# Optimization experiments

Measured on AMD Instinct MI355X. Metric: run time of the kernel, lower is better.

The kernel has to match this reference:

```python
import jax, jax.numpy as jnp
import numpy as np

NUM_LAYERS = 2
SHAPES = [(100, 100), (50, 50), (25, 25), (13, 13)]  # (H, W) per level
D, NH, NP, NL = 256, 8, 4, 4
DH = D // NH
DFF = 1024
B = 2
S = sum(h * w for h, w in SHAPES)  # 13294


def layer_norm(x, g, b, eps=1e-5):
    m = x.mean(-1, keepdims=True)
    v = jnp.var(x, axis=-1, keepdims=True)
    return (x - m) * jax.lax.rsqrt(v + eps) * g + b


def get_reference_points(valid_ratios):
    refs = []
    for lvl, (H_, W_) in enumerate(SHAPES):
        ry, rx = jnp.meshgrid(jnp.linspace(0.5, H_ - 0.5, H_),
                              jnp.linspace(0.5, W_ - 0.5, W_), indexing='ij')
        ry = ry.reshape(-1)[None] / (valid_ratios[:, None, lvl, 1] * H_)
        rx = rx.reshape(-1)[None] / (valid_ratios[:, None, lvl, 0] * W_)
        refs.append(jnp.stack([rx, ry], -1))
    ref = jnp.concatenate(refs, 1)                      # [B, S, 2]
    return ref[:, :, None] * valid_ratios[:, None]      # [B, S, NL, 2]


def sample_level(value_l, H_, W_, loc):
    # value_l: [B, nH, H*W, Dh]; loc: [B, Q, nH, P, 2] normalized in [0,1]
    x = loc[..., 0] * W_ - 0.5
    y = loc[..., 1] * H_ - 0.5
    x0 = jnp.floor(x)
    y0 = jnp.floor(y)
    Bq, Q = loc.shape[0], loc.shape[1]
    acc = 0.
    corners = ((x0, y0, (x0 + 1 - x) * (y0 + 1 - y)),
               (x0 + 1, y0, (x - x0) * (y0 + 1 - y)),
               (x0, y0 + 1, (x0 + 1 - x) * (y - y0)),
               (x0 + 1, y0 + 1, (x - x0) * (y - y0)))
    for xi, yi, w in corners:  # zero-padding grid_sample: invalid corners contribute 0
        valid = (xi >= 0) & (xi <= W_ - 1) & (yi >= 0) & (yi <= H_ - 1)
        idx = (jnp.clip(yi, 0, H_ - 1) * W_ + jnp.clip(xi, 0, W_ - 1)).astype(jnp.int32)
        idx = jnp.transpose(idx, (0, 2, 1, 3)).reshape(Bq, NH, Q * NP)
        g = jnp.take_along_axis(value_l, idx[..., None], axis=2)  # [B,nH,Q*P,Dh]
        wv = jnp.transpose((w * valid).astype(value_l.dtype), (0, 2, 1, 3)).reshape(Bq, NH, Q * NP)
        acc = acc + g * wv[..., None]
    return acc.reshape(Bq, NH, Q, NP, DH)


def msda(query, ref, src, W_val, b_val, W_off, b_off, W_attn, b_attn, W_out, b_out):
    Bq, Q = query.shape[:2]
    value = (src @ W_val + b_val).reshape(Bq, S, NH, DH)
    off = (query @ W_off + b_off).reshape(Bq, Q, NH, NL, NP, 2)
    attn = jax.nn.softmax((query @ W_attn + b_attn).reshape(Bq, Q, NH, NL * NP), -1)
    attn = attn.reshape(Bq, Q, NH, NL, NP)
    normalizer = jnp.array([[w, h] for h, w in SHAPES], dtype=query.dtype)  # [NL,2] (x,y)
    loc = ref[:, :, None, :, None, :] + off / normalizer[None, None, None, :, None, :]
    out = jnp.zeros((Bq, NH, Q, DH), query.dtype)
    start = 0
    for l, (H_, W_) in enumerate(SHAPES):
        v_l = jnp.transpose(value[:, start:start + H_ * W_], (0, 2, 1, 3))  # [B,nH,HW,Dh]
        samp = sample_level(v_l, H_, W_, loc[:, :, :, l])                    # [B,nH,Q,P,Dh]
        w_l = jnp.transpose(attn[:, :, :, l], (0, 2, 1, 3))                  # [B,nH,Q,P]
        out = out + (samp * w_l[..., None]).sum(3)
        start += H_ * W_
    out = jnp.transpose(out, (0, 2, 1, 3)).reshape(Bq, Q, D)
    return out @ W_out + b_out


def setup_inputs() -> dict:
    key = jax.random.key(0)
    ks = jax.random.split(key, 12)
    sc = 0.02
    inp = {
        'src': jax.random.normal(ks[0], (B, S, D), jnp.float32),
        'spatial_shapes': np.array(SHAPES, dtype=np.int64),
        'valid_ratios': jnp.ones((B, NL, 2), jnp.float32),
        'W_off': sc * jax.random.normal(ks[1], (NUM_LAYERS, D, NH * NL * NP * 2), jnp.float32),
        'b_off': jnp.zeros((NUM_LAYERS, NH * NL * NP * 2), jnp.float32),
        'W_attn': sc * jax.random.normal(ks[2], (NUM_LAYERS, D, NH * NL * NP), jnp.float32),
        'b_attn': jnp.zeros((NUM_LAYERS, NH * NL * NP), jnp.float32),
        'W_val': sc * jax.random.normal(ks[3], (NUM_LAYERS, D, D), jnp.float32),
        'b_val': jnp.zeros((NUM_LAYERS, D), jnp.float32),
        'W_out': sc * jax.random.normal(ks[4], (NUM_LAYERS, D, D), jnp.float32),
        'b_out': jnp.zeros((NUM_LAYERS, D), jnp.float32),
        'ln1_g': jnp.ones((NUM_LAYERS, D), jnp.float32),
        'ln1_b': jnp.zeros((NUM_LAYERS, D), jnp.float32),
        'W1': sc * jax.random.normal(ks[5], (NUM_LAYERS, D, DFF), jnp.float32),
        'b1': jnp.zeros((NUM_LAYERS, DFF), jnp.float32),
        'W2': sc * jax.random.normal(ks[6], (NUM_LAYERS, DFF, D), jnp.float32),
        'b2': jnp.zeros((NUM_LAYERS, D), jnp.float32),
        'ln2_g': jnp.ones((NUM_LAYERS, D), jnp.float32),
        'ln2_b': jnp.zeros((NUM_LAYERS, D), jnp.float32),
    }
    return inp


def reference(src, spatial_shapes, valid_ratios, W_off, b_off, W_attn, b_attn,
              W_val, b_val, W_out, b_out, ln1_g, ln1_b, W1, b1, W2, b2, ln2_g, ln2_b):
    # Deformable-DETR encoder stack (dropout=0 / eval mode, pos=None, no padding mask).
    ref = get_reference_points(valid_ratios)  # [B, S, NL, 2]
    x = src
    for i in range(NUM_LAYERS):
        x2 = msda(x, ref, x, W_val[i], b_val[i], W_off[i], b_off[i],
                  W_attn[i], b_attn[i], W_out[i], b_out[i])
        x = layer_norm(x + x2, ln1_g[i], ln1_b[i])
        h = jax.nn.relu(x @ W1[i] + b1[i]) @ W2[i] + b2[i]
        x = layer_norm(x + h, ln2_g[i], ln2_b[i])
    return x
```

## Files before the change

### kernel.cpp

```cpp
#include <hip/hip_runtime.h>
#include <math.h>


#define S_TOT 13294
#define BATCH 2
#define M_TOT (BATCH * S_TOT)
#define M_PAD 26624

typedef __attribute__((ext_vector_type(8))) short short8;
typedef __attribute__((ext_vector_type(4))) float floatx4;
typedef __attribute__((ext_vector_type(2))) float floatx2;

#define AS1C(p) ((const __attribute__((address_space(1))) void*)(p))
#define AS3(p)  ((__attribute__((address_space(3))) void*)(p))

static __device__ __forceinline__ unsigned short f2bf(float x) {
    union { float f; unsigned u; } v; v.f = x;
    unsigned r = v.u + 0x7FFFu + ((v.u >> 16) & 1u);
    return (unsigned short)(r >> 16);
}
static __device__ __forceinline__ float b2f(unsigned short u) {
    union { unsigned u; float f; } v; v.u = (unsigned)u << 16; return v.f;
}
static __device__ __forceinline__ float bflo(unsigned u) {
    union { unsigned u; float f; } v; v.u = u << 16; return v.f;
}
static __device__ __forceinline__ float bfhi(unsigned u) {
    union { unsigned u; float f; } v; v.u = u & 0xFFFF0000u; return v.f;
}
static __device__ __forceinline__ float braw(unsigned u) {
    union { unsigned u; float f; } v; v.u = u; return v.f;
}

template<int TM, bool RELU, bool BF16OUT, bool PROJ>
__global__ __launch_bounds__(256)
void mgemm(const unsigned short* __restrict__ A,
           const unsigned short* __restrict__ BT,
           const float* __restrict__ bias,
           const float* __restrict__ bias2,
           const float* __restrict__ bias3,
           unsigned short* __restrict__ Cb,
           unsigned short* __restrict__ Cb2,
           int M, int N, int K)
{
    constexpr int WM = (TM == 128) ? 2 : 1;
    constexpr int WN = 4 / WM;
    constexpr int MI = TM / (WM * 16);
    constexpr int NI = 128 / (WN * 16);
    __shared__ __align__(16) unsigned short smemA[2 * TM * 32];
    __shared__ __align__(16) unsigned short smemB[2 * 128 * 32];
    const int tid  = threadIdx.x;
    const int lane = tid & 63;
    const int w    = tid >> 6;
    const int wm   = w % WM, wn = w / WM;
    const int lr   = lane & 15, quad = lane >> 4;
    const int bm   = blockIdx.y * TM;
    const int bn   = blockIdx.x * 128;

    floatx4 acc[MI][NI];
    #pragma unroll
    for (int i = 0; i < MI; ++i)
        #pragma unroll
        for (int j = 0; j < NI; ++j)
            acc[i][j] = (floatx4){0.f, 0.f, 0.f, 0.f};

    const int srow = lane >> 2;
    const int selt = (lane & 3) << 3;

    for (int k0 = 0; k0 < K; k0 += 64) {
        #pragma unroll
        for (int c = 0; c < 2; ++c) {
            if (TM == 128) {
                #pragma unroll
                for (int jj = 0; jj < 2; ++jj) {
                    const int j = 2 * w + jj;
                    const unsigned short* ga = A  + (size_t)(bm + j * 16 + srow) * K + k0 + c * 32 + selt;
                    const unsigned short* gb = BT + (size_t)(bn + j * 16 + srow) * K + k0 + c * 32 + selt;
                    __builtin_amdgcn_global_load_lds(AS1C(ga), AS3(smemA + c * (TM * 32) + j * 512), 16, 0, 0);
                    __builtin_amdgcn_global_load_lds(AS1C(gb), AS3(smemB + c * 4096 + j * 512), 16, 0, 0);
                }
            } else {
                const unsigned short* ga = A + (size_t)(bm + w * 16 + srow) * K + k0 + c * 32 + selt;
                __builtin_amdgcn_global_load_lds(AS1C(ga), AS3(smemA + c * (TM * 32) + w * 512), 16, 0, 0);
                #pragma unroll
                for (int jj = 0; jj < 2; ++jj) {
                    const int j = 2 * w + jj;
                    const unsigned short* gb = BT + (size_t)(bn + j * 16 + srow) * K + k0 + c * 32 + selt;
                    __builtin_amdgcn_global_load_lds(AS1C(gb), AS3(smemB + c * 4096 + j * 512), 16, 0, 0);
                }
            }
        }
        __syncthreads();

        #pragma unroll
        for (int c = 0; c < 2; ++c) {
            short8 av[MI], bv[NI];
            #pragma unroll
            for (int mi = 0; mi < MI; ++mi)
                av[mi] = *(const short8*)&smemA[c * (TM * 32) + (wm * MI * 16 + mi * 16 + lr) * 32 + quad * 8];
            #pragma unroll
            for (int ni = 0; ni < NI; ++ni)
                bv[ni] = *(const short8*)&smemB[c * 4096 + (wn * NI * 16 + ni * 16 + lr) * 32 + quad * 8];
            #pragma unroll
            for (int mi = 0; mi < MI; ++mi)
                #pragma unroll
                for (int ni = 0; ni < NI; ++ni)
                    acc[mi][ni] = __builtin_amdgcn_mfma_f32_16x16x32_bf16(
                        av[mi], bv[ni], acc[mi][ni], 0, 0, 0);
        }
        __syncthreads();
    }

    #pragma unroll
    for (int mi = 0; mi < MI; ++mi) {
        #pragma unroll
        for (int ni = 0; ni < NI; ++ni) {
            #pragma unroll
            for (int r = 0; r < 4; ++r) {
                const int row = bm + wm * MI * 16 + mi * 16 + quad * 4 + r;
                const int col = bn + wn * NI * 16 + ni * 16 + lr;
                if (PROJ) {
                    const float bb = (col < 256) ? bias[col]
                                   : (col < 512) ? bias2[col - 256]
                                                 : bias3[col - 512];
                    const float v = acc[mi][ni][r] + bb;
                    if (col < 256) Cb[(size_t)row * 256 + col] = f2bf(v);
                    else           Cb2[(size_t)row * 384 + (col - 256)] = f2bf(v);
                } else {
                    float v = acc[mi][ni][r] + bias[col];
                    if (RELU) v = fmaxf(v, 0.0f);
                    if (BF16OUT) Cb[(size_t)row * N + col] = f2bf(v);
                }
            }
        }
    }
}

template<bool HASF, bool HASB>
__global__ __launch_bounds__(512)
void mgemm_ln(const unsigned short* __restrict__ A,
              const unsigned short* __restrict__ BT,
              const float* __restrict__ bias,
              const unsigned short* __restrict__ R,
              const float* __restrict__ g,
              const float* __restrict__ beta,
              float* __restrict__ outF,
              unsigned short* __restrict__ outB,
              int M, int K)
{
    __shared__ __align__(16) unsigned short smemA[2 * 4096];
    __shared__ __align__(16) unsigned short smemB[2 * 16384];
    const int lane = threadIdx.x & 63;
    const int w    = threadIdx.x >> 6;
    const int lr   = lane & 15, quad = lane >> 4;
    const int bm   = blockIdx.x * 64;
    const int srow = lane >> 2;
    const int selt = (lane & 3) << 3;

    floatx4 acc[4][2];
    #pragma unroll
    for (int i = 0; i < 4; ++i)
        #pragma unroll
        for (int j = 0; j < 2; ++j)
            acc[i][j] = (floatx4){0.f, 0.f, 0.f, 0.f};

    auto stage = [&](int kt, int buf) {
        const int k0 = kt * 64;
        {
            const int c = w & 1, j = w >> 1;
            const unsigned short* ga = A + (size_t)(bm + j * 16 + srow) * K + k0 + c * 32 + selt;
            __builtin_amdgcn_global_load_lds(AS1C(ga), AS3(smemA + buf * 4096 + c * 2048 + j * 512), 16, 0, 0);
        }
        #pragma unroll
        for (int c = 0; c < 2; ++c) {
            #pragma unroll
            for (int jj = 0; jj < 2; ++jj) {
                const int j = w * 2 + jj;
                const unsigned short* gb = BT + (size_t)(j * 16 + srow) * K + k0 + c * 32 + selt;
                __builtin_amdgcn_global_load_lds(AS1C(gb), AS3(smemB + buf * 16384 + c * 8192 + j * 512), 16, 0, 0);
            }
        }
    };

    const int NK = K >> 6;
    stage(0, 0);
    for (int kt = 0; kt < NK; ++kt) {
        const int buf = kt & 1;
        __syncthreads();
        if (kt + 1 < NK) stage(kt + 1, buf ^ 1);
        #pragma unroll
        for (int c = 0; c < 2; ++c) {
            short8 av[4], bv[2];
            #pragma unroll
            for (int mi = 0; mi < 4; ++mi)
                av[mi] = *(const short8*)&smemA[buf * 4096 + c * 2048 + (mi * 16 + lr) * 32 + quad * 8];
            #pragma unroll
            for (int ni = 0; ni < 2; ++ni)
                bv[ni] = *(const short8*)&smemB[buf * 16384 + c * 8192 + (w * 32 + ni * 16 + lr) * 32 + quad * 8];
            #pragma unroll
            for (int mi = 0; mi < 4; ++mi)
                #pragma unroll
                for (int ni = 0; ni < 2; ++ni)
                    acc[mi][ni] = __builtin_amdgcn_mfma_f32_16x16x32_bf16(
                        av[mi], bv[ni], acc[mi][ni], 0, 0, 0);
        }
    }

    float bs[2], gs[2], bts[2];
    #pragma unroll
    for (int ni = 0; ni < 2; ++ni) {
        const int col = w * 32 + ni * 16 + lr;
        bs[ni] = bias[col]; gs[ni] = g[col]; bts[ni] = beta[col];
    }
    float* lnbuf = (float*)smemA;

    #pragma unroll
    for (int mi = 0; mi < 4; ++mi) {
        #pragma unroll
        for (int r = 0; r < 4; ++r) {
            const int rl = mi * 16 + quad * 4 + r;
            const int grow = bm + rl;
            const bool act = grow < M;
            float p = 0.f, q = 0.f;
            #pragma unroll
            for (int ni = 0; ni < 2; ++ni) {
                const int col = w * 32 + ni * 16 + lr;
                const float rv = act ? b2f(R[(size_t)grow * 256 + col]) : 0.f;
                const float x = acc[mi][ni][r] + bs[ni] + rv;
                acc[mi][ni][r] = x;
                p += x; q += x * x;
            }
            #pragma unroll
            for (int o = 1; o < 16; o <<= 1) {
                p += __shfl_xor(p, o, 64);
                q += __shfl_xor(q, o, 64);
            }
            if (lr == 0) {
                lnbuf[rl * 16 + 2 * w]     = p;
                lnbuf[rl * 16 + 2 * w + 1] = q;
            }
        }
    }
    __syncthreads();
    #pragma unroll
    for (int mi = 0; mi < 4; ++mi) {
        #pragma unroll
        for (int r = 0; r < 4; ++r) {
            const int rl = mi * 16 + quad * 4 + r;
            const int grow = bm + rl;
            const float4 pa = *(const float4*)&lnbuf[rl * 16];
            const float4 pb = *(const float4*)&lnbuf[rl * 16 + 4];
            const float4 pc = *(const float4*)&lnbuf[rl * 16 + 8];
            const float4 pd = *(const float4*)&lnbuf[rl * 16 + 12];
            const float s  = pa.x + pa.z + pb.x + pb.z + pc.x + pc.z + pd.x + pd.z;
            const float s2 = pa.y + pa.w + pb.y + pb.w + pc.y + pc.w + pd.y + pd.w;
            const float mean = s * (1.0f / 256.0f);
            const float var  = s2 * (1.0f / 256.0f) - mean * mean;
            const float rs   = rsqrtf(var + 1e-5f);
            if (grow < M) {
                #pragma unroll
                for (int ni = 0; ni < 2; ++ni) {
                    const int col = w * 32 + ni * 16 + lr;
                    const float y = (acc[mi][ni][r] - mean) * rs * gs[ni] + bts[ni];
                    if (HASF) outF[(size_t)grow * 256 + col] = y;
                    if (HASB) outB[(size_t)grow * 256 + col] = f2bf(y);
                }
            }
        }
    }
}

__global__ __launch_bounds__(256)
void convpad(const float* __restrict__ X, unsigned short* __restrict__ Y, int M)
{
    const int idx = blockIdx.x * 256 + threadIdx.x;
    const int row = idx >> 6;
    const int c4  = (idx & 63) << 2;
    if (row >= M_PAD) return;
    float4 v = {0.f, 0.f, 0.f, 0.f};
    if (row < M) v = ((const float4*)(X + (size_t)row * 256))[c4 >> 2];
    unsigned p0 = (unsigned)f2bf(v.x) | ((unsigned)f2bf(v.y) << 16);
    unsigned p1 = (unsigned)f2bf(v.z) | ((unsigned)f2bf(v.w) << 16);
    uint2 o; o.x = p0; o.y = p1;
    *(uint2*)(Y + (size_t)row * 256 + c4) = o;
}

struct WJobs {
    const float* W[12];
    unsigned short* WT[12];
    int K[12], N[12], tx[12], start[12];
};

__global__ __launch_bounds__(256)
void wtrans_all(WJobs jb)
{
    __shared__ float t[32][33];
    const int bx = blockIdx.x;
    int seg = 0;
    #pragma unroll
    for (int s = 1; s < 12; ++s) if (bx >= jb.start[s]) seg = s;
    const float* W = jb.W[seg];
    unsigned short* WT = jb.WT[seg];
    const int K = jb.K[seg], N = jb.N[seg], tx = jb.tx[seg];
    const int local = bx - jb.start[seg];
    const int n0 = (local % tx) * 32, k0 = (local / tx) * 32;
    const int c = threadIdx.x & 31, r0 = threadIdx.x >> 5;
    #pragma unroll
    for (int rr = r0; rr < 32; rr += 8)
        t[rr][c] = W[(size_t)(k0 + rr) * N + n0 + c];
    __syncthreads();
    #pragma unroll
    for (int rr = r0; rr < 32; rr += 8)
        WT[(size_t)(n0 + rr) * K + k0 + c] = f2bf(t[c][rr]);
}

__global__ __launch_bounds__(256)
void msda_kernel(const unsigned short* __restrict__ valb,
                 const unsigned short* __restrict__ oab,
                 const float* __restrict__ vr,
                 unsigned short* __restrict__ out)
{
    __shared__ __align__(16) char smeta[8 * 128 * 32];
    const int t = threadIdx.x;
    const int bid = (blockIdx.x & 7) * 416 + (blockIdx.x >> 3);

    {
        const int wv = t >> 6, lane = t & 63;
        const int lqA = wv * 2 + (lane >> 5);
        const int bq = bid * 8 + lqA;
        const int h = (lane >> 2) & 7;
        const int j = lane & 3;
        if (bq < M_TOT) {
            const int b = (bq >= S_TOT) ? 1 : 0;
            const int q = bq - b * S_TOT;
            const int bofs = b * (S_TOT * 512);
            int Hq, rr, cc, lq;
            if (q < 10000)      { lq = 0; Hq = 100; rr = q / 100;              cc = q - rr * 100; }
            else if (q < 12500) { lq = 1; Hq = 50;  int r2 = q - 10000; rr = r2 / 50; cc = r2 - rr * 50; }
            else if (q < 13125) { lq = 2; Hq = 25;  int r2 = q - 12500; rr = r2 / 25; cc = r2 - rr * 25; }
            else                { lq = 3; Hq = 13;  int r2 = q - 13125; rr = r2 / 13; cc = r2 - rr * 13; }
            const float rxb = (cc + 0.5f) / (vr[(b * 4 + lq) * 2 + 0] * (float)Hq);
            const float ryb = (rr + 0.5f) / (vr[(b * 4 + lq) * 2 + 1] * (float)Hq);
            const int HWt[4] = {100, 50, 25, 13};
            const int stt[4] = {0, 10000, 12500, 13125};
            const int HW = HWt[j], st = stt[j];
            const float fW = (float)HW;
            const float refxw = rxb * vr[(b * 4 + j) * 2 + 0] * fW - 0.5f;
            const float refyw = ryb * vr[(b * 4 + j) * 2 + 1] * fW - 0.5f;
            const unsigned short* row = oab + (size_t)bq * 384;
            const uint2 lgu = *(const uint2*)(row + 256 + h * 16 + j * 4);
            const float l0 = bflo(lgu.x), l1 = bfhi(lgu.x);
            const float l2 = bflo(lgu.y), l3 = bfhi(lgu.y);
            float mx = fmaxf(fmaxf(l0, l1), fmaxf(l2, l3));
            mx = fmaxf(mx, __shfl_xor(mx, 1, 64));
            mx = fmaxf(mx, __shfl_xor(mx, 2, 64));
            const float e0 = __expf(l0 - mx), e1 = __expf(l1 - mx);
            const float e2 = __expf(l2 - mx), e3 = __expf(l3 - mx);
            float ss = e0 + e1 + e2 + e3;
            ss += __shfl_xor(ss, 1, 64);
            ss += __shfl_xor(ss, 2, 64);
            const float inv = 1.0f / ss;
            const uint4 ou = *(const uint4*)(row + h * 32 + j * 8);
            const float oxs[4] = {bflo(ou.x), bflo(ou.y), bflo(ou.z), bflo(ou.w)};
            const float oys[4] = {bfhi(ou.x), bfhi(ou.y), bfhi(ou.z), bfhi(ou.w)};
            const float aw[4]  = {e0 * inv, e1 * inv, e2 * inv, e3 * inv};
            char* mb = smeta + (size_t)(lqA * 128 + h * 16 + j * 4) * 32;
            const int swz = ((h * 4 + j) & 7) << 4;
            #pragma unroll
            for (int p = 0; p < 4; ++p) {
                const float x = refxw + oxs[p];
                const float y = refyw + oys[p];
                const float x0f = floorf(x), y0f = floorf(y);
                const int x0 = (int)x0f, y0 = (int)y0f;
                const float fx = x - x0f, fy = y - y0f;
                const float wb[4] = {(1.f - fx) * (1.f - fy), fx * (1.f - fy),
                                     (1.f - fx) * fy,         fx * fy};
                const int xs[2] = {x0, x0 + 1};
                const int ys2[2] = {y0, y0 + 1};
                int iv[4]; float wv4[4];
                #pragma unroll
                for (int k = 0; k < 4; ++k) {
                    const int xi = xs[k & 1], yi = ys2[k >> 1];
                    const bool vld = ((unsigned)xi < (unsigned)HW) && ((unsigned)yi < (unsigned)HW);
                    const int xc = min(max(xi, 0), HW - 1);
                    const int yc = min(max(yi, 0), HW - 1);
                    iv[k] = bofs + ((st + yc * HW + xc) << 9) + (h << 6);
                    wv4[k] = vld ? wb[k] * aw[p] : 0.0f;
                }
                int4 i4; i4.x = iv[0]; i4.y = iv[1]; i4.z = iv[2]; i4.w = iv[3];
                float4 w4; w4.x = wv4[0]; w4.y = wv4[1]; w4.z = wv4[2]; w4.w = wv4[3];
                *(int4*)(mb + ((p * 32) ^ swz)) = i4;
                *(float4*)(mb + ((p * 32 + 16) ^ swz)) = w4;
            }
        }
    }
    __syncthreads();
    {
        const int lq2 = t >> 5;
        const int r = t & 31;
        const int h2 = r >> 2;
        const int cg = r & 3;
        const int bq2 = bid * 8 + lq2;
        if (bq2 < M_TOT) {
            const char* vbase = (const char*)valb;
            const unsigned cgo = cg * 16;
            floatx2 a0 = {0.f, 0.f}, a1 = {0.f, 0.f}, a2 = {0.f, 0.f}, a3 = {0.f, 0.f};
            const char* mb2 = smeta + (size_t)(lq2 * 128 + h2 * 16) * 32;
            #pragma unroll 4
            for (int s = 0; s < 16; ++s) {
                const int swz2 = ((h2 * 4 + (s >> 2)) & 7) << 4;
                const int4  iv = *(const int4*)(mb2 + ((s * 32) ^ swz2));
                const float4 w4 = *(const float4*)(mb2 + ((s * 32 + 16) ^ swz2));
                const uint4 u0 = *(const uint4*)(vbase + (unsigned)(iv.x + cgo));
                const uint4 u1 = *(const uint4*)(vbase + (unsigned)(iv.y + cgo));
                const uint4 u2 = *(const uint4*)(vbase + (unsigned)(iv.z + cgo));
                const uint4 u3 = *(const uint4*)(vbase + (unsigned)(iv.w + cgo));
                #define ACC8(UU, WW) { \
                    const floatx2 w2 = {WW, WW}; \
                    const floatx2 t0 = {bflo(UU.x), braw(UU.x)}; \
                    const floatx2 t1 = {bflo(UU.y), braw(UU.y)}; \
                    const floatx2 t2 = {bflo(UU.z), braw(UU.z)}; \
                    const floatx2 t3 = {bflo(UU.w), braw(UU.w)}; \
                    a0 += w2 * t0; a1 += w2 * t1; a2 += w2 * t2; a3 += w2 * t3; }
                ACC8(u0, w4.x) ACC8(u1, w4.y) ACC8(u2, w4.z) ACC8(u3, w4.w)
                #undef ACC8
            }
            uint4 o;
            o.x = (unsigned)f2bf(a0.x) | ((unsigned)f2bf(a0.y) << 16);
            o.y = (unsigned)f2bf(a1.x) | ((unsigned)f2bf(a1.y) << 16);
            o.z = (unsigned)f2bf(a2.x) | ((unsigned)f2bf(a2.y) << 16);
            o.w = (unsigned)f2bf(a3.x) | ((unsigned)f2bf(a3.y) << 16);
            *(uint4*)(out + (size_t)bq2 * 256 + h2 * 32 + cg * 8) = o;
        }
    }
}

extern "C" void kernel_launch(void* const* d_in, const int* in_sizes, int n_in,
                              void* d_out, int out_size, void* d_ws, size_t ws_size,
                              hipStream_t stream)
{
    const float* src    = (const float*)d_in[0];
    const float* vr     = (const float*)d_in[2];
    const float* W_off  = (const float*)d_in[3];
    const float* b_off  = (const float*)d_in[4];
    const float* W_attn = (const float*)d_in[5];
    const float* b_attn = (const float*)d_in[6];
    const float* W_val  = (const float*)d_in[7];
    const float* b_val  = (const float*)d_in[8];
    const float* W_out  = (const float*)d_in[9];
    const float* b_out  = (const float*)d_in[10];
    const float* ln1_g  = (const float*)d_in[11];
    const float* ln1_b  = (const float*)d_in[12];
    const float* W1     = (const float*)d_in[13];
    const float* b1     = (const float*)d_in[14];
    const float* W2     = (const float*)d_in[15];
    const float* b2     = (const float*)d_in[16];
    const float* ln2_g  = (const float*)d_in[17];
    const float* ln2_b  = (const float*)d_in[18];
    float* out = (float*)d_out;

    const int M = M_TOT;

    char* wsb = (char*)d_ws;
    unsigned short* HBF  = (unsigned short*)wsb;
    unsigned short* OAB  = (unsigned short*)wsb;
    unsigned short* VALB = (unsigned short*)(wsb + 20447232);
    unsigned short* X1B  = (unsigned short*)(wsb + 54525952);
    unsigned short* RB   = (unsigned short*)(wsb + 81788928);
    unsigned short* YBF  = (unsigned short*)(wsb + 95420416);
    unsigned short* WT   = (unsigned short*)(wsb + 109051904);

    const size_t LWT = 753664;
    const size_t oProj = 0, oOut = 163840, oW1 = 229376, oW2 = 491520;

    WJobs jb;
    int startAcc = 0;
    for (int i = 0; i < 2; ++i) {
        unsigned short* wt = WT + i * LWT;
        const float* srcs[6] = {W_val + i * 65536, W_off + i * 65536, W_attn + i * 32768,
                                W_out + i * 65536, W1 + i * 262144, W2 + i * 262144};
        unsigned short* dsts[6] = {wt + oProj, wt + oProj + 65536, wt + oProj + 131072,
                                   wt + oOut, wt + oW1, wt + oW2};
        const int Ks[6] = {256, 256, 256, 256, 256, 1024};
        const int Ns[6] = {256, 256, 128, 256, 1024, 256};
        for (int s = 0; s < 6; ++s) {
            const int idx = i * 6 + s;
            jb.W[idx] = srcs[s]; jb.WT[idx] = dsts[s];
            jb.K[idx] = Ks[s]; jb.N[idx] = Ns[s]; jb.tx[idx] = Ns[s] / 32;
            jb.start[idx] = startAcc;
            startAcc += (Ns[s] / 32) * (Ks[s] / 32);
        }
    }
    wtrans_all<<<dim3(startAcc), 256, 0, stream>>>(jb);

    const int GM128 = M_PAD / 128;
    const int GM64  = M_PAD / 64;
    const dim3 blk(256);
    const dim3 blk512(512);

    for (int i = 0; i < 2; ++i) {
        unsigned short* wt = WT + i * LWT;

        if (i == 0)
            convpad<<<dim3(M_PAD / 4), blk, 0, stream>>>(src, RB, M);

        mgemm<64, false, false, true><<<dim3(5, GM64), blk, 0, stream>>>(
            RB, wt + oProj, b_val + i * 256, b_off + i * 256, b_attn + i * 128,
            VALB, OAB, M, 640, 256);

        msda_kernel<<<dim3(3328), blk, 0, stream>>>(VALB, OAB, vr, YBF);

        mgemm_ln<false, true><<<dim3(GM64), blk512, 0, stream>>>(
            YBF, wt + oOut, b_out + i * 256, RB,
            ln1_g + i * 256, ln1_b + i * 256, nullptr, X1B, M, 256);

        mgemm<128, true, true, false><<<dim3(8, GM128), blk, 0, stream>>>(
            X1B, wt + oW1, b1 + i * 1024, nullptr, nullptr,
            HBF, nullptr, M, 1024, 256);

        if (i == 0)
            mgemm_ln<false, true><<<dim3(GM64), blk512, 0, stream>>>(
                HBF, wt + oW2, b2 + i * 256, X1B,
                ln2_g + i * 256, ln2_b + i * 256, nullptr, RB, M, 1024);
        else
            mgemm_ln<true, false><<<dim3(GM64), blk512, 0, stream>>>(
                HBF, wt + oW2, b2 + i * 256, X1B,
                ln2_g + i * 256, ln2_b + i * 256, out, nullptr, M, 1024);
    }
}
```

Before: 422.3 us.

## Single-buffer LDS with XOR swizzle in GEMM+LayerNorm kernel

Replaces the double-buffered LDS staging in the mgemm_ln kernel with a single buffer. Global-to-LDS loads now use an XOR-swizzled source column, and the MFMA fragment reads apply the matching swizzle to avoid LDS bank conflicts. Halving LDS usage may allow more resident blocks per CU. In exchange, loads no longer overlap compute and each k-step needs an extra barrier.

```diff
diff --git a/kernel.cpp b/kernel.cpp
--- a/kernel.cpp
+++ b/kernel.cpp
@@ -148,14 +148,14 @@
               unsigned short* __restrict__ outB,
               int M, int K)
 {
-    __shared__ __align__(16) unsigned short smemA[2 * 4096];
-    __shared__ __align__(16) unsigned short smemB[2 * 16384];
+    __shared__ __align__(16) unsigned short smemA[4096];
+    __shared__ __align__(16) unsigned short smemB[16384];
     const int lane = threadIdx.x & 63;
     const int w    = threadIdx.x >> 6;
     const int lr   = lane & 15, quad = lane >> 4;
     const int bm   = blockIdx.x * 64;
     const int srow = lane >> 2;
-    const int selt = (lane & 3) << 3;
+    const int sw   = (((lane & 3) ^ (srow & 3)) << 3);
 
     floatx4 acc[4][2];
     #pragma unroll
@@ -164,39 +164,38 @@
         for (int j = 0; j < 2; ++j)
             acc[i][j] = (floatx4){0.f, 0.f, 0.f, 0.f};
 
-    auto stage = [&](int kt, int buf) {
-        const int k0 = kt * 64;
+    const int NK = K >> 6;
+    for (int kt = 0; kt < NK; ++kt) {
+        const int k0 = kt << 6;
         {
             const int c = w & 1, j = w >> 1;
-            const unsigned short* ga = A + (size_t)(bm + j * 16 + srow) * K + k0 + c * 32 + selt;
-            __builtin_amdgcn_global_load_lds(AS1C(ga), AS3(smemA + buf * 4096 + c * 2048 + j * 512), 16, 0, 0);
+            const unsigned short* ga = A + (size_t)(bm + j * 16 + srow) * K + k0 + c * 32 + sw;
+            __builtin_amdgcn_global_load_lds(AS1C(ga), AS3(smemA + c * 2048 + j * 512), 16, 0, 0);
         }
         #pragma unroll
         for (int c = 0; c < 2; ++c) {
             #pragma unroll
             for (int jj = 0; jj < 2; ++jj) {
                 const int j = w * 2 + jj;
-                const unsigned short* gb = BT + (size_t)(j * 16 + srow) * K + k0 + c * 32 + selt;
-                __builtin_amdgcn_global_load_lds(AS1C(gb), AS3(smemB + buf * 16384 + c * 8192 + j * 512), 16, 0, 0);
-            }
-        }
-    };
-
-    const int NK = K >> 6;
-    stage(0, 0);
-    for (int kt = 0; kt < NK; ++kt) {
-        const int buf = kt & 1;
+                const unsigned short* gb = BT + (size_t)(j * 16 + srow) * K + k0 + c * 32 + sw;
+                __builtin_amdgcn_global_load_lds(AS1C(gb), AS3(smemB + c * 8192 + j * 512), 16, 0, 0);
+            }
+        }
         __syncthreads();
-        if (kt + 1 < NK) stage(kt + 1, buf ^ 1);
+
         #pragma unroll
         for (int c = 0; c < 2; ++c) {
             short8 av[4], bv[2];
             #pragma unroll
-            for (int mi = 0; mi < 4; ++mi)
-                av[mi] = *(const short8*)&smemA[buf * 4096 + c * 2048 + (mi * 16 + lr) * 32 + quad * 8];
-            #pragma unroll
-            for (int ni = 0; ni < 2; ++ni)
-                bv[ni] = *(const short8*)&smemB[buf * 16384 + c * 8192 + (w * 32 + ni * 16 + lr) * 32 + quad * 8];
+            for (int mi = 0; mi < 4; ++mi) {
+                const int row = mi * 16 + lr;
+                av[mi] = *(const short8*)&smemA[c * 2048 + row * 32 + ((quad ^ (row & 3)) << 3)];
+            }
+            #pragma unroll
+            for (int ni = 0; ni < 2; ++ni) {
+                const int col = w * 32 + ni * 16 + lr;
+                bv[ni] = *(const short8*)&smemB[c * 8192 + col * 32 + ((quad ^ (col & 3)) << 3)];
+            }
             #pragma unroll
             for (int mi = 0; mi < 4; ++mi)
                 #pragma unroll
@@ -204,6 +203,7 @@
                     acc[mi][ni] = __builtin_amdgcn_mfma_f32_16x16x32_bf16(
                         av[mi], bv[ni], acc[mi][ni], 0, 0, 0);
         }
+        __syncthreads();
     }
 
     float bs[2], gs[2], bts[2];
```

Result: slower. 431.0 us (+2.1%).
